# Kernel tuning notes

Measured on AMD Instinct MI355X. Metric: run time of the kernel, lower is better.

The kernel has to match this reference:

```python
import jax, jax.numpy as jnp
import numpy as np

D = 512          # d_model
DS = 32          # d_state
EXPAND = 2
HEADDIM = 64
R = 4            # mimo_rank
DIN = EXPAND * D             # 1024 inner dim
H = DIN // HEADDIM           # 16 heads
DFF = ((int(D * 8 / 3) + 7) // 8) * 8  # 1368 SwiGLU hidden
CHUNK = max(1, 64 // R)      # 16
BATCH, SEQ = 4, 512


def setup_inputs() -> dict:
    key = jax.random.key(0)
    ks = jax.random.split(key, 12)
    def w(k, shape, fan):
        return jax.random.normal(k, shape, jnp.float32) / np.float32(np.sqrt(fan))
    return {
        "x": jax.random.normal(ks[0], (BATCH, SEQ, D), jnp.float32),
        "mask": jnp.ones((BATCH, SEQ), jnp.float32),
        "norm1_w": jnp.ones((D,), jnp.float32),
        "norm2_w": jnp.ones((D,), jnp.float32),
        "Wz": w(ks[1], (D, DIN), D),
        "Wx": w(ks[2], (D, DIN), D),
        "Wb": w(ks[3], (D, H * R * DS), D),
        "Wc": w(ks[4], (D, H * R * DS), D),
        "Wdt": w(ks[5], (D, H), D),
        "dt_bias": jnp.zeros((H,), jnp.float32),
        "A_log": jnp.log(jnp.arange(1, H + 1, dtype=jnp.float32)),
        "D_skip": jnp.ones((H,), jnp.float32),
        "Wout": w(ks[6], (DIN, D), DIN),
        "w1": w(ks[7], (D, DFF), D),
        "w2": w(ks[8], (DFF, D), DFF),
        "w3": w(ks[9], (D, DFF), D),
    }


def rmsnorm(x, wgt, eps=1e-6):
    rms = jnp.sqrt(jnp.mean(x * x, axis=-1, keepdims=True) + eps)
    return x / rms * wgt


def ssm_mixer(x, Wz, Wx, Wb, Wc, Wdt, dt_bias, A_log, D_skip, Wout):
    # x: [B, S, D] (already masked)
    B, S, _ = x.shape
    pad = (CHUNK - S % CHUNK) % CHUNK
    if pad > 0:
        x = jnp.pad(x, ((0, 0), (0, pad), (0, 0)))
    Sp = x.shape[1]
    z = x @ Wz                                        # [B,Sp,DIN] gate
    u = (x @ Wx).reshape(B, Sp, H, HEADDIM)           # [B,Sp,H,P]
    Bm = (x @ Wb).reshape(B, Sp, H, R, DS)            # [B,Sp,H,R,N]
    Cm = (x @ Wc).reshape(B, Sp, H, R, DS)
    dt = jax.nn.softplus(x @ Wdt + dt_bias)           # [B,Sp,H]
    a = jnp.exp(dt * (-jnp.exp(A_log)))               # per-step decay [B,Sp,H]
    ud = u * dt[..., None]                            # discretized input

    def step(h, inp):
        a_t, B_t, C_t, ud_t = inp                     # [B,H], [B,H,R,N], [B,H,R,N], [B,H,P]
        h = a_t[:, :, None, None, None] * h + jnp.einsum('bhrn,bhp->bhrnp', B_t, ud_t)
        y = jnp.einsum('bhrn,bhrnp->bhp', C_t, h)
        return h, y

    h0 = jnp.zeros((B, H, R, DS, HEADDIM), x.dtype)
    xs = (a.swapaxes(0, 1), Bm.swapaxes(0, 1), Cm.swapaxes(0, 1), ud.swapaxes(0, 1))
    _, ys = jax.lax.scan(step, h0, xs)                # ys: [Sp,B,H,P]
    y = ys.swapaxes(0, 1) + u * D_skip[None, None, :, None]
    y = y.reshape(B, Sp, DIN) * jax.nn.silu(z)
    y = y @ Wout                                      # [B,Sp,D]
    return y[:, :S]


def reference(x, mask, norm1_w, norm2_w, Wz, Wx, Wb, Wc, Wdt, dt_bias,
              A_log, D_skip, Wout, w1, w2, w3):
    m = mask[..., None]
    xn = rmsnorm(x, norm1_w) * m
    y = ssm_mixer(xn, Wz, Wx, Wb, Wc, Wdt, dt_bias, A_log, D_skip, Wout) * m
    x = x + y
    xn2 = rmsnorm(x, norm2_w)
    x = x + (jax.nn.silu(xn2 @ w1) * (xn2 @ w3)) @ w2
    return x * m
```

## Files before the change

### kernel.cpp

```cpp
#include <hip/hip_runtime.h>
#include <hip/hip_bf16.h>
#include <math.h>

#define Bn 4
#define Sn 512
#define Dn 512
#define DINn 1024
#define Hn 16
#define Pn 64
#define RNn 128
#define DFFn 1368
#define KP2 1408
#define BSn (Bn*Sn)
#define CH 64
#define NCH (Sn/CH)
#define PSTR 6144
#define FPAD 2816
#define NSCAN (Bn*NCH*Hn)

typedef __attribute__((ext_vector_type(8))) short short8;
typedef __attribute__((ext_vector_type(4))) float f32x4;
typedef __attribute__((ext_vector_type(4))) short short4v;

static __device__ __forceinline__ float bf2f(__hip_bfloat16 v){return __bfloat162float(v);}
static __device__ __forceinline__ __hip_bfloat16 f2bf(float v){return __float2bfloat16(v);}
static __device__ __forceinline__ short f2bfs(float v){ __hip_bfloat16 b=f2bf(v); short s; __builtin_memcpy(&s,&b,2); return s; }
static __device__ __forceinline__ float bfs2f(short s){ __hip_bfloat16 b; __builtin_memcpy(&b,&s,2); return bf2f(b); }

typedef const __attribute__((address_space(1))) unsigned int* gas1_u32p;
typedef __attribute__((address_space(3))) unsigned int* gas3_u32p;
static __device__ __forceinline__ void gl_lds16(const void* g, void* l) {
  __builtin_amdgcn_global_load_lds((gas1_u32p)g, (gas3_u32p)l, 16, 0, 0);
}

struct T8 {
  const float* src[8];
  __hip_bfloat16* dst[8];
  int Rr[8], Cc[8], RrPad[8], CcPad[8], gw[8];
  int start[9];
};

static __device__ __forceinline__ void transpose_tile(const T8& d, int bid, int t,
                                                      float (*tile)[65]) {
  int i = 0;
#pragma unroll
  for (int k = 1; k < 8; ++k) if (bid >= d.start[k]) i = k;
  int rel = bid - d.start[i];
  int gx = rel % d.gw[i], gy = rel / d.gw[i];
  const float* in = d.src[i];
  __hip_bfloat16* out = d.dst[i];
  int Rr = d.Rr[i], Cc = d.Cc[i], RrPad = d.RrPad[i], CcPad = d.CcPad[i];
  int tx = t & 15, ty = t >> 4;
#pragma unroll
  for (int i4 = 0; i4 < 4; ++i4) {
    int r = gy * 64 + ty + i4 * 16;
    int c0 = gx * 64 + tx * 4;
    f32x4 v = (f32x4){0.f, 0.f, 0.f, 0.f};
    if (r < Rr && c0 + 3 < Cc) v = *(const f32x4*)(in + (size_t)r * Cc + c0);
    tile[ty + i4 * 16][tx * 4 + 0] = v[0];
    tile[ty + i4 * 16][tx * 4 + 1] = v[1];
    tile[ty + i4 * 16][tx * 4 + 2] = v[2];
    tile[ty + i4 * 16][tx * 4 + 3] = v[3];
  }
  __syncthreads();
#pragma unroll
  for (int i4 = 0; i4 < 4; ++i4) {
    int r2 = gx * 64 + ty + i4 * 16;
    int c2 = gy * 64 + tx * 4;
    if (r2 < CcPad && c2 + 3 < RrPad) {
      int k = ty + i4 * 16;
      short4v o;
      o.x = f2bfs(tile[tx * 4 + 0][k]);
      o.y = f2bfs(tile[tx * 4 + 1][k]);
      o.z = f2bfs(tile[tx * 4 + 2][k]);
      o.w = f2bfs(tile[tx * 4 + 3][k]);
      *(short4v*)((short*)out + (size_t)r2 * RrPad + c2) = o;
    }
  }
}

__global__ __launch_bounds__(256) void prep_kernel(
    T8 d, const float* __restrict__ x, const float* __restrict__ w,
    const float* __restrict__ mask, const float* __restrict__ Wdt,
    const float* __restrict__ dtb, const float* __restrict__ Alog,
    __hip_bfloat16* __restrict__ outb, float* __restrict__ dt,
    float* __restrict__ la, float* __restrict__ rs, int tstart) {
  __shared__ float tile[64][65];
  __shared__ float xs[Dn];
  __shared__ float red[4];
  int bid = blockIdx.x, t = threadIdx.x;
  if (bid < tstart) {
    transpose_tile(d, bid, t, tile);
  } else if (bid - tstart < BSn) {
    int row = bid - tstart;
    const float* xr = x + (size_t)row * Dn;
    float v0 = xr[t], v1 = xr[t + 256];
    float ss = v0 * v0 + v1 * v1;
#pragma unroll
    for (int o = 32; o > 0; o >>= 1) ss += __shfl_down(ss, o);
    if ((t & 63) == 0) red[t >> 6] = ss;
    __syncthreads();
    float tot = red[0] + red[1] + red[2] + red[3];
    float sc = rsqrtf(tot * (1.f / Dn) + 1e-6f) * mask[row];
    float o0 = v0 * sc * w[t], o1v = v1 * sc * w[t + 256];
    outb[(size_t)row * Dn + t] = f2bf(o0);
    outb[(size_t)row * Dn + t + 256] = f2bf(o1v);
    xs[t] = o0;
    xs[t + 256] = o1v;
    __syncthreads();
    int h = t >> 4, j = t & 15;
    float s = 0.f;
#pragma unroll
    for (int kk = 0; kk < 32; ++kk) {
      int k = j + kk * 16;
      s = fmaf(xs[k], Wdt[k * Hn + h], s);
    }
#pragma unroll
    for (int o = 8; o > 0; o >>= 1) s += __shfl_down(s, o, 16);
    if (j == 0) {
      float v = s + dtb[h];
      float sp = (v > 20.f) ? v : log1pf(expf(v));
      float Ah = expf(Alog[h]);
      dt[(size_t)row * Hn + h] = sp;
      la[(size_t)row * Hn + h] = -Ah * sp;
    }
  } else {
    *(f32x4*)&rs[t * 8]     = (f32x4){0.f, 0.f, 0.f, 0.f};
    *(f32x4*)&rs[t * 8 + 4] = (f32x4){0.f, 0.f, 0.f, 0.f};
  }
}

__global__ __launch_bounds__(256) void gemm_kernel(
    const __hip_bfloat16* __restrict__ A, const __hip_bfloat16* __restrict__ BT,
    __hip_bfloat16* __restrict__ C, int M, int N, int K) {
  __shared__ short As[2][4096];
  __shared__ short Bs[2][4096];
  int m0 = blockIdx.x * 128, n0 = blockIdx.y * 128;
  int t = threadIdx.x;
  int lane = t & 63, wv = t >> 6;
  int wm = (wv & 1) * 64, wn = (wv >> 1) * 64;
  f32x4 acc[4][4];
#pragma unroll
  for (int i = 0; i < 4; ++i)
#pragma unroll
    for (int j = 0; j < 4; ++j) acc[i][j] = (f32x4){0.f, 0.f, 0.f, 0.f};
  const short* Ag = (const short*)A;
  const short* Bg = (const short*)BT;
  int r0 = t >> 2, p = t & 3;
  int q0 = (p - (r0 >> 1)) & 3;
  int r1 = r0 + 64;
  int q1 = (p - (r1 >> 1)) & 3;
  const short* Asrc0 = Ag + (size_t)(m0 + r0) * K + 8 * q0;
  const short* Asrc1 = Ag + (size_t)(m0 + r1) * K + 8 * q1;
  const short* Bsrc0 = Bg + (size_t)(n0 + r0) * K + 8 * q0;
  const short* Bsrc1 = Bg + (size_t)(n0 + r1) * K + 8 * q1;
  int fr = lane & 15, fq = lane >> 4;
  int kTiles = K >> 5;
  auto stage = [&](int buf, int k0) {
    gl_lds16(Asrc0 + k0, &As[buf][wv * 512]);
    gl_lds16(Asrc1 + k0, &As[buf][2048 + wv * 512]);
    gl_lds16(Bsrc0 + k0, &Bs[buf][wv * 512]);
    gl_lds16(Bsrc1 + k0, &Bs[buf][2048 + wv * 512]);
  };
  auto domfma = [&](int buf) {
    short8 af[4], bfr[4];
#pragma unroll
    for (int i = 0; i < 4; ++i) {
      int rr = wm + i * 16 + fr;
      af[i] = *(const short8*)&As[buf][rr * 32 + (((rr >> 1) + fq) & 3) * 8];
    }
#pragma unroll
    for (int i = 0; i < 4; ++i) {
      int rr = wn + i * 16 + fr;
      bfr[i] = *(const short8*)&Bs[buf][rr * 32 + (((rr >> 1) + fq) & 3) * 8];
    }
#pragma unroll
    for (int mi = 0; mi < 4; ++mi)
#pragma unroll
      for (int ni = 0; ni < 4; ++ni)
        acc[mi][ni] = __builtin_amdgcn_mfma_f32_16x16x32_bf16(af[mi], bfr[ni], acc[mi][ni], 0, 0, 0);
  };
  stage(0, 0);
  for (int kt = 0; kt < kTiles; ++kt) {
    int buf = kt & 1;
    __syncthreads();
    if (kt + 1 < kTiles) stage(buf ^ 1, (kt + 1) << 5);
    domfma(buf);
  }
  int fq4 = (lane >> 4) * 4;
#pragma unroll
  for (int mi = 0; mi < 4; ++mi)
#pragma unroll
    for (int ni = 0; ni < 4; ++ni) {
      int col = n0 + wn + ni * 16 + fr;
      if (col < N) {
        int rowb = m0 + wm + mi * 16 + fq4;
#pragma unroll
        for (int r = 0; r < 4; ++r)
          C[(size_t)(rowb + r) * N + col] = f2bf(acc[mi][ni][r]);
      }
    }
}

template <int MODE>
__global__ __launch_bounds__(256) void gemm64_ep_kernel(
    const __hip_bfloat16* __restrict__ A, const __hip_bfloat16* __restrict__ BT,
    const float* __restrict__ aux, const float* __restrict__ mask,
    float* __restrict__ out, float* __restrict__ rs, int M, int N, int K) {
  __shared__ short As[2][64][72];
  __shared__ short Bs[2][64][72];
  int m0 = blockIdx.x * 64, n0 = blockIdx.y * 64;
  int t = threadIdx.x;
  int lane = t & 63, wv = t >> 6;
  int wm = (wv & 1) * 32, wn = (wv >> 1) * 32;
  f32x4 acc[2][2];
#pragma unroll
  for (int i = 0; i < 2; ++i)
#pragma unroll
    for (int j = 0; j < 2; ++j) acc[i][j] = (f32x4){0.f, 0.f, 0.f, 0.f};
  const short* Ag = (const short*)A;
  const short* Bg = (const short*)BT;
  int sr = t >> 2;
  int sc = (t & 3) * 16;
  const short* Ap = Ag + (size_t)(m0 + sr) * K + sc;
  const short* Bp = Bg + (size_t)(n0 + sr) * K + sc;
  int fr = lane & 15, fq = (lane >> 4) * 8;
  int kTiles = K >> 6;
  short8 a0A = 0, a1A = 0, b0A = 0, b1A = 0;
  short8 a0B = 0, a1B = 0, b0B = 0, b1B = 0;
  auto loadA = [&](int k0) {
    a0A = *(const short8*)(Ap + k0);
    a1A = *(const short8*)(Ap + k0 + 8);
    b0A = *(const short8*)(Bp + k0);
    b1A = *(const short8*)(Bp + k0 + 8);
  };
  auto loadB = [&](int k0) {
    a0B = *(const short8*)(Ap + k0);
    a1B = *(const short8*)(Ap + k0 + 8);
    b0B = *(const short8*)(Bp + k0);
    b1B = *(const short8*)(Bp + k0 + 8);
  };
  auto storeA = [&](int buf) {
    *(short8*)&As[buf][sr][sc] = a0A;
    *(short8*)&As[buf][sr][sc + 8] = a1A;
    *(short8*)&Bs[buf][sr][sc] = b0A;
    *(short8*)&Bs[buf][sr][sc + 8] = b1A;
  };
  auto storeB = [&](int buf) {
    *(short8*)&As[buf][sr][sc] = a0B;
    *(short8*)&As[buf][sr][sc + 8] = a1B;
    *(short8*)&Bs[buf][sr][sc] = b0B;
    *(short8*)&Bs[buf][sr][sc + 8] = b1B;
  };
  auto mfma = [&](int buf) {
#pragma unroll
    for (int kk = 0; kk < 2; ++kk) {
      short8 af[2], bfr[2];
#pragma unroll
      for (int i = 0; i < 2; ++i) af[i] = *(const short8*)&As[buf][wm + i * 16 + fr][kk * 32 + fq];
#pragma unroll
      for (int i = 0; i < 2; ++i) bfr[i] = *(const short8*)&Bs[buf][wn + i * 16 + fr][kk * 32 + fq];
#pragma unroll
      for (int mi = 0; mi < 2; ++mi)
#pragma unroll
        for (int ni = 0; ni < 2; ++ni)
          acc[mi][ni] = __builtin_amdgcn_mfma_f32_16x16x32_bf16(af[mi], bfr[ni], acc[mi][ni], 0, 0, 0);
    }
  };
  loadA(0);
  storeA(0);
  loadA(64);
  __syncthreads();
  for (int kt = 0; kt < kTiles; kt += 2) {
    storeA(1);
    if (kt + 2 < kTiles) loadB((kt + 2) << 6);
    mfma(0);
    __syncthreads();
    if (kt + 2 < kTiles) storeB(0);
    if (kt + 3 < kTiles) loadA((kt + 3) << 6);
    mfma(1);
    __syncthreads();
  }
  int fq4 = (lane >> 4) * 4;
  float rsum[2][4];
#pragma unroll
  for (int mi = 0; mi < 2; ++mi)
#pragma unroll
    for (int r = 0; r < 4; ++r) rsum[mi][r] = 0.f;
#pragma unroll
  for (int mi = 0; mi < 2; ++mi)
#pragma unroll
    for (int ni = 0; ni < 2; ++ni) {
      int col = n0 + wn + ni * 16 + fr;
#pragma unroll
      for (int r = 0; r < 4; ++r) {
        int row = m0 + wm + mi * 16 + fq4 + r;
        float m = mask[row];
        size_t a = (size_t)row * N + col;
        float v = acc[mi][ni][r];
        if (MODE == 1) {
          float ov = aux[a] + v * m;
          out[a] = ov;
          rsum[mi][r] += ov * ov;
        } else {
          out[a] = (aux[a] + v) * m;
        }
      }
    }
  if (MODE == 1) {
#pragma unroll
    for (int mi = 0; mi < 2; ++mi)
#pragma unroll
      for (int r = 0; r < 4; ++r) {
        float s = rsum[mi][r];
#pragma unroll
        for (int o = 8; o > 0; o >>= 1) s += __shfl_xor(s, o);
        if ((lane & 15) == 0) {
          int row = m0 + wm + mi * 16 + fq4 + r;
          atomicAdd(&rs[row], s);
        }
      }
  }
}

__global__ __launch_bounds__(256) void gemm64g_kernel(
    const float* __restrict__ X, const float* __restrict__ rs,
    const float* __restrict__ n2w, const __hip_bfloat16* __restrict__ BT,
    __hip_bfloat16* __restrict__ G, int M, int K) {
  __shared__ short As[2][64][72];
  __shared__ short B1s[2][64][72];
  __shared__ short B3s[2][64][72];
  __shared__ float ssc[64];
  __shared__ float sw[Dn];
  int m0 = blockIdx.x * 64, n0 = blockIdx.y * 64;
  int t = threadIdx.x;
  int lane = t & 63, wv = t >> 6;
  int wm = (wv & 1) * 32, wn = (wv >> 1) * 32;
  f32x4 acc1[2][2], acc3[2][2];
#pragma unroll
  for (int i = 0; i < 2; ++i)
#pragma unroll
    for (int j = 0; j < 2; ++j) {
      acc1[i][j] = (f32x4){0.f, 0.f, 0.f, 0.f};
      acc3[i][j] = (f32x4){0.f, 0.f, 0.f, 0.f};
    }
  const short* Bg = (const short*)BT;
  int sr = t >> 2;
  int sc = (t & 3) * 16;
  const float* Xp  = X + (size_t)(m0 + sr) * Dn + sc;
  const short* B1p = Bg + (size_t)(n0 + sr) * K + sc;
  const short* B3p = Bg + (size_t)(DFFn + n0 + sr) * K + sc;
  int fr = lane & 15, fq = (lane >> 4) * 8;
  int kTiles = K >> 6;
  if (t < 64) ssc[t] = rsqrtf(rs[m0 + t] * (1.f / Dn) + 1e-6f);
  sw[t] = n2w[t];
  sw[t + 256] = n2w[t + 256];
  __syncthreads();
  float scl = ssc[sr];
  short8 a0A = 0, a1A = 0, c0A = 0, c1A = 0, d0A = 0, d1A = 0;
  short8 a0B = 0, a1B = 0, c0B = 0, c1B = 0, d0B = 0, d1B = 0;
  auto cvtA = [&](int k0, short8& lo, short8& hi) {
    f32x4 v[4];
#pragma unroll
    for (int q = 0; q < 4; ++q) v[q] = *(const f32x4*)(Xp + k0 + q * 4);
    short tmp[16];
#pragma unroll
    for (int q = 0; q < 4; ++q)
#pragma unroll
      for (int jj = 0; jj < 4; ++jj)
        tmp[q * 4 + jj] = f2bfs(v[q][jj] * scl * sw[k0 + sc + q * 4 + jj]);
    __builtin_memcpy(&lo, tmp, 16);
    __builtin_memcpy(&hi, tmp + 8, 16);
  };
  auto loadA = [&](int k0) {
    cvtA(k0, a0A, a1A);
    c0A = *(const short8*)(B1p + k0);
    c1A = *(const short8*)(B1p + k0 + 8);
    d0A = *(const short8*)(B3p + k0);
    d1A = *(const short8*)(B3p + k0 + 8);
  };
  auto loadB = [&](int k0) {
    cvtA(k0, a0B, a1B);
    c0B = *(const short8*)(B1p + k0);
    c1B = *(const short8*)(B1p + k0 + 8);
    d0B = *(const short8*)(B3p + k0);
    d1B = *(const short8*)(B3p + k0 + 8);
  };
  auto storeA = [&](int buf) {
    *(short8*)&As[buf][sr][sc] = a0A;
    *(short8*)&As[buf][sr][sc + 8] = a1A;
    *(short8*)&B1s[buf][sr][sc] = c0A;
    *(short8*)&B1s[buf][sr][sc + 8] = c1A;
    *(short8*)&B3s[buf][sr][sc] = d0A;
    *(short8*)&B3s[buf][sr][sc + 8] = d1A;
  };
  auto storeB = [&](int buf) {
    *(short8*)&As[buf][sr][sc] = a0B;
    *(short8*)&As[buf][sr][sc + 8] = a1B;
    *(short8*)&B1s[buf][sr][sc] = c0B;
    *(short8*)&B1s[buf][sr][sc + 8] = c1B;
    *(short8*)&B3s[buf][sr][sc] = d0B;
    *(short8*)&B3s[buf][sr][sc + 8] = d1B;
  };
  auto mfma = [&](int buf) {
#pragma unroll
    for (int kk = 0; kk < 2; ++kk) {
      short8 af[2], b1f[2], b3f[2];
#pragma unroll
      for (int i = 0; i < 2; ++i) af[i]  = *(const short8*)&As[buf][wm + i * 16 + fr][kk * 32 + fq];
#pragma unroll
      for (int i = 0; i < 2; ++i) b1f[i] = *(const short8*)&B1s[buf][wn + i * 16 + fr][kk * 32 + fq];
#pragma unroll
      for (int i = 0; i < 2; ++i) b3f[i] = *(const short8*)&B3s[buf][wn + i * 16 + fr][kk * 32 + fq];
#pragma unroll
      for (int mi = 0; mi < 2; ++mi)
#pragma unroll
        for (int ni = 0; ni < 2; ++ni) {
          acc1[mi][ni] = __builtin_amdgcn_mfma_f32_16x16x32_bf16(af[mi], b1f[ni], acc1[mi][ni], 0, 0, 0);
          acc3[mi][ni] = __builtin_amdgcn_mfma_f32_16x16x32_bf16(af[mi], b3f[ni], acc3[mi][ni], 0, 0, 0);
        }
    }
  };
  loadA(0);
  storeA(0);
  loadA(64);
  __syncthreads();
  for (int kt = 0; kt < kTiles; kt += 2) {
    storeA(1);
    if (kt + 2 < kTiles) loadB((kt + 2) << 6);
    mfma(0);
    __syncthreads();
    if (kt + 2 < kTiles) storeB(0);
    if (kt + 3 < kTiles) loadA((kt + 3) << 6);
    mfma(1);
    __syncthreads();
  }
  int fq4 = (lane >> 4) * 4;
#pragma unroll
  for (int mi = 0; mi < 2; ++mi)
#pragma unroll
    for (int ni = 0; ni < 2; ++ni) {
      int col = n0 + wn + ni * 16 + fr;
      bool valid = col < DFFn;
#pragma unroll
      for (int r = 0; r < 4; ++r) {
        int row = m0 + wm + mi * 16 + fq4 + r;
        float h1v = acc1[mi][ni][r];
        float sil = h1v / (1.f + __expf(-h1v));
        float g = sil * acc3[mi][ni][r];
        G[(size_t)row * KP2 + col] = valid ? f2bf(g) : f2bf(0.f);
      }
    }
}

__global__ __launch_bounds__(256) void chunk_intra_kernel(
    const __hip_bfloat16* __restrict__ P, const float* __restrict__ dt,
    const float* __restrict__ la, __hip_bfloat16* __restrict__ ysb,
    __hip_bfloat16* __restrict__ Sbuf, float* __restrict__ ecL, float* __restrict__ ec) {
  int id = blockIdx.x;
  int h = id & 15, c = (id >> 4) & 7, b = id >> 7;
  int t = threadIdx.x, lane = t & 63, wv = t >> 6;
  __shared__ __align__(16) char smem[55040];
  short* sCB = (short*)smem;
  short* sB  = (short*)(smem + 18432);
  short* sUD = (short*)(smem + 35840);
  short* sG  = (short*)(smem + 45056);
  float* scum = (float*)(smem + 54272);
  float* sws  = scum + 64;
  float* sdt  = sws + 64;
  int row0 = b * Sn + c * CH;
  const short* Pb = (const short*)P;
#pragma unroll
  for (int i = 0; i < 4; ++i) {
    int idx = t + i * 256;
    int r = idx >> 4, kk = (idx & 15) * 8;
    *(short8*)&sCB[r * 136 + kk] = *(const short8*)(Pb + (size_t)(row0 + r) * PSTR + 4096 + h * 128 + kk);
    *(short8*)&sB [r * 136 + kk] = *(const short8*)(Pb + (size_t)(row0 + r) * PSTR + 2048 + h * 128 + kk);
  }
  if (t < 64) { sdt[t] = dt[(size_t)(row0 + t) * Hn + h]; scum[t] = la[(size_t)(row0 + t) * Hn + h]; }
  __syncthreads();
  if (wv == 0) {
    float v = scum[lane];
#pragma unroll
    for (int o = 1; o < 64; o <<= 1) { float n = __shfl_up(v, o); if (lane >= o) v += n; }
    scum[lane] = v;
    float c63 = __shfl(v, 63);
    sws[lane] = __expf(c63 - v);
    ec[((size_t)((b * NCH + c) * Hn + h)) * 64 + lane] = __expf(v);
    if (lane == 0) ecL[(b * NCH + c) * Hn + h] = __expf(c63);
  }
#pragma unroll
  for (int i = 0; i < 2; ++i) {
    int idx = t + i * 256;
    int s = idx >> 3, pc = (idx & 7) * 8;
    short8 uv = *(const short8*)(Pb + (size_t)(row0 + s) * PSTR + 1024 + h * 64 + pc);
    float dv = sdt[s];
#pragma unroll
    for (int j = 0; j < 8; ++j) sUD[(pc + j) * 72 + s] = f2bfs(bfs2f(uv[j]) * dv);
  }
  __syncthreads();
  int fr = lane & 15, fq = (lane >> 4) * 8, q4 = (lane >> 4) * 4;
  {
    short8 af[4];
#pragma unroll
    for (int k = 0; k < 4; ++k) af[k] = *(short8*)&sCB[(16 * wv + fr) * 136 + k * 32 + fq];
#pragma unroll
    for (int j = 0; j < 4; ++j) {
      f32x4 acc = (f32x4){0.f, 0.f, 0.f, 0.f};
#pragma unroll
      for (int k = 0; k < 4; ++k) {
        short8 bf = *(short8*)&sB[(16 * j + fr) * 136 + k * 32 + fq];
        acc = __builtin_amdgcn_mfma_f32_16x16x32_bf16(af[k], bf, acc, 0, 0, 0);
      }
      int ss = 16 * j + fr;
      float cs = scum[ss];
#pragma unroll
      for (int r = 0; r < 4; ++r) {
        int tt = 16 * wv + q4 + r;
        float w = (ss <= tt) ? __expf(scum[tt] - cs) : 0.f;
        sG[tt * 72 + ss] = f2bfs(acc[r] * w);
      }
    }
  }
  __syncthreads();
#pragma unroll
  for (int i = 0; i < 32; ++i) {
    int idx = t + i * 256;
    int rn = idx >> 6, s = idx & 63;
    sCB[rn * 72 + s] = f2bfs(bfs2f(sB[s * 136 + rn]) * sws[s]);
  }
  __syncthreads();
  {
    short8 ag[2];
#pragma unroll
    for (int k = 0; k < 2; ++k) ag[k] = *(short8*)&sG[(16 * wv + fr) * 72 + k * 32 + fq];
#pragma unroll
    for (int j = 0; j < 4; ++j) {
      f32x4 acc = (f32x4){0.f, 0.f, 0.f, 0.f};
#pragma unroll
      for (int k = 0; k < 2; ++k) {
        short8 bf = *(short8*)&sUD[(16 * j + fr) * 72 + k * 32 + fq];
        acc = __builtin_amdgcn_mfma_f32_16x16x32_bf16(ag[k], bf, acc, 0, 0, 0);
      }
#pragma unroll
      for (int r = 0; r < 4; ++r)
        ysb[(size_t)(row0 + 16 * wv + q4 + r) * DINn + h * 64 + 16 * j + fr] = f2bf(acc[r]);
    }
  }
#pragma unroll
  for (int mt0 = 0; mt0 < 2; ++mt0) {
    int mt = wv * 2 + mt0;
    short8 ab[2];
#pragma unroll
    for (int k = 0; k < 2; ++k) ab[k] = *(short8*)&sCB[(16 * mt + fr) * 72 + k * 32 + fq];
#pragma unroll
    for (int j = 0; j < 4; ++j) {
      f32x4 acc = (f32x4){0.f, 0.f, 0.f, 0.f};
#pragma unroll
      for (int k = 0; k < 2; ++k) {
        short8 bf = *(short8*)&sUD[(16 * j + fr) * 72 + k * 32 + fq];
        acc = __builtin_amdgcn_mfma_f32_16x16x32_bf16(ab[k], bf, acc, 0, 0, 0);
      }
      int pp = 16 * j + fr;
      int rn0 = 16 * mt + q4;
      short4v o;
      o.x = f2bfs(acc[0]); o.y = f2bfs(acc[1]); o.z = f2bfs(acc[2]); o.w = f2bfs(acc[3]);
      *(short4v*)&((short*)Sbuf)[((size_t)((b * NCH + c) * Hn + h) * 64 + pp) * 128 + rn0] = o;
    }
  }
}

__global__ __launch_bounds__(256) void inter_gate_kernel(
    const __hip_bfloat16* __restrict__ P, const __hip_bfloat16* __restrict__ Sbuf,
    const float* __restrict__ ecL, const float* __restrict__ ec,
    const __hip_bfloat16* __restrict__ ysb, const float* __restrict__ Dsk,
    __hip_bfloat16* __restrict__ y2b) {
  int id = blockIdx.x;
  int h = id & 15, c = (id >> 4) & 7, b = id >> 7;
  int t = threadIdx.x, lane = t & 63, wv = t >> 6;
  __shared__ __align__(16) short sC[64 * 136];
  __shared__ __align__(16) short sHt[64 * 136];
  __shared__ __align__(16) short sz[64 * 64];
  __shared__ __align__(16) short su[64 * 64];
  __shared__ float sec[64];
  int row0 = b * Sn + c * CH;
  const short* Pb = (const short*)P;
#pragma unroll
  for (int i = 0; i < 2; ++i) {
    int idx = t + i * 256;
    int r = idx >> 3, pc = (idx & 7) * 8;
    *(short8*)&sz[r * 64 + pc] = *(const short8*)(Pb + (size_t)(row0 + r) * PSTR + h * 64 + pc);
    *(short8*)&su[r * 64 + pc] = *(const short8*)(Pb + (size_t)(row0 + r) * PSTR + 1024 + h * 64 + pc);
  }
  if (c > 0) {
#pragma unroll
    for (int i = 0; i < 4; ++i) {
      int idx = t + i * 256;
      int r = idx >> 4, kk = (idx & 15) * 8;
      *(short8*)&sC[r * 136 + kk] = *(const short8*)(Pb + (size_t)(row0 + r) * PSTR + 4096 + h * 128 + kk);
    }
    float wch[8];
    {
      float w = 1.f;
      for (int cp = c - 1; cp >= 0; --cp) {
        wch[cp] = w;
        if (cp > 0) w *= ecL[(size_t)((b * NCH + cp) * Hn + h)];
      }
    }
    float hacc[32];
#pragma unroll
    for (int jj = 0; jj < 32; ++jj) hacc[jj] = 0.f;
    const short* Sb = (const short*)Sbuf;
    for (int cp = 0; cp < c; ++cp) {
      size_t base = ((size_t)((b * NCH + cp) * Hn + h)) * 8192 + (size_t)t * 32;
      float wv2 = wch[cp];
#pragma unroll
      for (int v4 = 0; v4 < 4; ++v4) {
        short8 sv = *(const short8*)(Sb + base + v4 * 8);
#pragma unroll
        for (int jj = 0; jj < 8; ++jj)
          hacc[v4 * 8 + jj] = fmaf(wv2, bfs2f(sv[jj]), hacc[v4 * 8 + jj]);
      }
    }
    int p = t >> 2, rn0 = (t & 3) * 32;
#pragma unroll
    for (int v4 = 0; v4 < 4; ++v4) {
      short8 o;
#pragma unroll
      for (int jj = 0; jj < 8; ++jj) o[jj] = f2bfs(hacc[v4 * 8 + jj]);
      *(short8*)&sHt[p * 136 + rn0 + v4 * 8] = o;
    }
    if (t < 64) sec[t] = ec[((size_t)((b * NCH + c) * Hn + h)) * 64 + t];
  }
  __syncthreads();
  int fr = lane & 15, fq = (lane >> 4) * 8, q4 = (lane >> 4) * 4;
  f32x4 acc[4];
#pragma unroll
  for (int j = 0; j < 4; ++j) acc[j] = (f32x4){0.f, 0.f, 0.f, 0.f};
  if (c > 0) {
    short8 af[4];
#pragma unroll
    for (int k = 0; k < 4; ++k) af[k] = *(short8*)&sC[(16 * wv + fr) * 136 + k * 32 + fq];
#pragma unroll
    for (int j = 0; j < 4; ++j)
#pragma unroll
      for (int k = 0; k < 4; ++k) {
        short8 bf = *(short8*)&sHt[(16 * j + fr) * 136 + k * 32 + fq];
        acc[j] = __builtin_amdgcn_mfma_f32_16x16x32_bf16(af[k], bf, acc[j], 0, 0, 0);
      }
  }
  float dsk = Dsk[h];
#pragma unroll
  for (int j = 0; j < 4; ++j) {
    int col = 16 * j + fr;
#pragma unroll
    for (int r = 0; r < 4; ++r) {
      int tt = 16 * wv + q4 + r;
      size_t a = (size_t)(row0 + tt) * DINn + h * 64 + col;
      float val = bf2f(ysb[a]);
      if (c > 0) val += sec[tt] * acc[j][r];
      float uu = bfs2f(su[tt * 64 + col]);
      float zz = bfs2f(sz[tt * 64 + col]);
      float sil = zz / (1.f + __expf(-zz));
      y2b[a] = f2bf((val + uu * dsk) * sil);
    }
  }
}

extern "C" void kernel_launch(void* const* d_in, const int* in_sizes, int n_in,
                              void* d_out, int out_size, void* d_ws, size_t ws_size,
                              hipStream_t stream) {
  const float* x    = (const float*)d_in[0];
  const float* mask = (const float*)d_in[1];
  const float* n1w  = (const float*)d_in[2];
  const float* n2w  = (const float*)d_in[3];
  const float* Wz   = (const float*)d_in[4];
  const float* Wx   = (const float*)d_in[5];
  const float* Wb   = (const float*)d_in[6];
  const float* Wc   = (const float*)d_in[7];
  const float* Wdt  = (const float*)d_in[8];
  const float* dtb  = (const float*)d_in[9];
  const float* Alog = (const float*)d_in[10];
  const float* Dsk  = (const float*)d_in[11];
  const float* Wout = (const float*)d_in[12];
  const float* w1   = (const float*)d_in[13];
  const float* w2   = (const float*)d_in[14];
  const float* w3   = (const float*)d_in[15];

  char* ws = (char*)d_ws;
  size_t off = 0;
  auto alloc = [&](size_t bytes) {
    char* p = ws + off;
    off += (bytes + 255) & ~(size_t)255;
    return p;
  };
  __hip_bfloat16* xnb = (__hip_bfloat16*)alloc((size_t)BSn * Dn * 2);
  __hip_bfloat16* P = (__hip_bfloat16*)alloc((size_t)BSn * PSTR * 2);
  float* dt  = (float*)alloc((size_t)BSn * Hn * 4);
  float* la  = (float*)alloc((size_t)BSn * Hn * 4);
  __hip_bfloat16* ysb = (__hip_bfloat16*)alloc((size_t)BSn * DINn * 2);
  float* ecL = (float*)alloc((size_t)Bn * NCH * Hn * 4);
  float* ec  = (float*)alloc((size_t)Bn * NCH * Hn * 64 * 4);
  float* rs  = (float*)alloc((size_t)BSn * 4);
  __hip_bfloat16* WallT = (__hip_bfloat16*)alloc((size_t)PSTR * Dn * 2);
  __hip_bfloat16* WoutT = (__hip_bfloat16*)alloc((size_t)Dn * DINn * 2);
  __hip_bfloat16* w13T  = (__hip_bfloat16*)alloc((size_t)FPAD * Dn * 2);
  __hip_bfloat16* w2T   = (__hip_bfloat16*)alloc((size_t)Dn * KP2 * 2);
  char* arena = alloc(22000000);
  __hip_bfloat16* Sbuf = (__hip_bfloat16*)arena;
  __hip_bfloat16* y2b  = (__hip_bfloat16*)(arena + 16777216);
  float* xres          = (float*)arena;
  __hip_bfloat16* gatedb = (__hip_bfloat16*)(arena + 4194304);

  T8 td;
  td.src[0] = Wz;   td.dst[0] = WallT;                      td.Rr[0] = 512;  td.Cc[0] = 1024; td.RrPad[0] = 512;  td.CcPad[0] = 1024;
  td.src[1] = Wx;   td.dst[1] = WallT + (size_t)1024 * 512; td.Rr[1] = 512;  td.Cc[1] = 1024; td.RrPad[1] = 512;  td.CcPad[1] = 1024;
  td.src[2] = Wb;   td.dst[2] = WallT + (size_t)2048 * 512; td.Rr[2] = 512;  td.Cc[2] = 2048; td.RrPad[2] = 512;  td.CcPad[2] = 2048;
  td.src[3] = Wc;   td.dst[3] = WallT + (size_t)4096 * 512; td.Rr[3] = 512;  td.Cc[3] = 2048; td.RrPad[3] = 512;  td.CcPad[3] = 2048;
  td.src[4] = Wout; td.dst[4] = WoutT;                      td.Rr[4] = 1024; td.Cc[4] = 512;  td.RrPad[4] = 1024; td.CcPad[4] = 512;
  td.src[5] = w1;   td.dst[5] = w13T;                       td.Rr[5] = 512;  td.Cc[5] = 1368; td.RrPad[5] = 512;  td.CcPad[5] = 1368;
  td.src[6] = w3;   td.dst[6] = w13T + (size_t)1368 * 512;  td.Rr[6] = 512;  td.Cc[6] = 1368; td.RrPad[6] = 512;  td.CcPad[6] = 1448;
  td.src[7] = w2;   td.dst[7] = w2T;                        td.Rr[7] = 1368; td.Cc[7] = 512;  td.RrPad[7] = KP2;  td.CcPad[7] = 512;
  int tot = 0;
  for (int i = 0; i < 8; ++i) {
    td.gw[i] = (td.CcPad[i] + 63) / 64;
    int gh = (td.RrPad[i] + 63) / 64;
    td.start[i] = tot;
    tot += td.gw[i] * gh;
  }
  td.start[8] = tot;

  prep_kernel<<<tot + BSn + 1, 256, 0, stream>>>(td, x, n1w, mask, Wdt, dtb, Alog, xnb, dt, la, rs, tot);
  gemm_kernel<<<dim3(16, 48), 256, 0, stream>>>(xnb, WallT, P, BSn, PSTR, Dn);
  chunk_intra_kernel<<<NSCAN, 256, 0, stream>>>(P, dt, la, ysb, Sbuf, ecL, ec);
  inter_gate_kernel<<<NSCAN, 256, 0, stream>>>(P, Sbuf, ecL, ec, ysb, Dsk, y2b);
  gemm64_ep_kernel<1><<<dim3(32, 8), 256, 0, stream>>>(y2b, WoutT, x, mask, xres, rs, BSn, Dn, DINn);
  gemm64g_kernel<<<dim3(32, KP2 / 64), 256, 0, stream>>>(xres, rs, n2w, w13T, gatedb, BSn, Dn);
  gemm64_ep_kernel<2><<<dim3(32, 8), 256, 0, stream>>>(gatedb, w2T, xres, mask, (float*)d_out, rs, BSn, Dn, KP2);
}
```

Baseline: 212.6 us.

## Fuse chunk scan kernels with flag-based inter-chunk sync and fold norm2 weight into W13

```diff
diff --git a/kernel.cpp b/kernel.cpp
--- a/kernel.cpp
+++ b/kernel.cpp
@@ -35,6 +35,7 @@
 
 struct T8 {
   const float* src[8];
+  const float* svec[8];
   __hip_bfloat16* dst[8];
   int Rr[8], Cc[8], RrPad[8], CcPad[8], gw[8];
   int start[9];
@@ -48,6 +49,7 @@
   int rel = bid - d.start[i];
   int gx = rel % d.gw[i], gy = rel / d.gw[i];
   const float* in = d.src[i];
+  const float* sv = d.svec[i];
   __hip_bfloat16* out = d.dst[i];
   int Rr = d.Rr[i], Cc = d.Cc[i], RrPad = d.RrPad[i], CcPad = d.CcPad[i];
   int tx = t & 15, ty = t >> 4;
@@ -69,11 +71,15 @@
     int c2 = gy * 64 + tx * 4;
     if (r2 < CcPad && c2 + 3 < RrPad) {
       int k = ty + i4 * 16;
+      float s0 = sv ? sv[c2 + 0] : 1.f;
+      float s1 = sv ? sv[c2 + 1] : 1.f;
+      float s2 = sv ? sv[c2 + 2] : 1.f;
+      float s3 = sv ? sv[c2 + 3] : 1.f;
       short4v o;
-      o.x = f2bfs(tile[tx * 4 + 0][k]);
-      o.y = f2bfs(tile[tx * 4 + 1][k]);
-      o.z = f2bfs(tile[tx * 4 + 2][k]);
-      o.w = f2bfs(tile[tx * 4 + 3][k]);
+      o.x = f2bfs(tile[tx * 4 + 0][k] * s0);
+      o.y = f2bfs(tile[tx * 4 + 1][k] * s1);
+      o.z = f2bfs(tile[tx * 4 + 2][k] * s2);
+      o.w = f2bfs(tile[tx * 4 + 3][k] * s3);
       *(short4v*)((short*)out + (size_t)r2 * RrPad + c2) = o;
     }
   }
@@ -84,7 +90,8 @@
     const float* __restrict__ mask, const float* __restrict__ Wdt,
     const float* __restrict__ dtb, const float* __restrict__ Alog,
     __hip_bfloat16* __restrict__ outb, float* __restrict__ dt,
-    float* __restrict__ la, float* __restrict__ rs, int tstart) {
+    float* __restrict__ la, float* __restrict__ rs, int* __restrict__ flags,
+    int tstart) {
   __shared__ float tile[64][65];
   __shared__ float xs[Dn];
   __shared__ float red[4];
@@ -127,6 +134,8 @@
   } else {
     *(f32x4*)&rs[t * 8]     = (f32x4){0.f, 0.f, 0.f, 0.f};
     *(f32x4*)&rs[t * 8 + 4] = (f32x4){0.f, 0.f, 0.f, 0.f};
+    ((int2*)flags)[t] = make_int2(0, 0);
+    if (t < 4) flags[512 + t] = 0;
   }
 }
 
@@ -206,7 +215,8 @@
 __global__ __launch_bounds__(256) void gemm64_ep_kernel(
     const __hip_bfloat16* __restrict__ A, const __hip_bfloat16* __restrict__ BT,
     const float* __restrict__ aux, const float* __restrict__ mask,
-    float* __restrict__ out, float* __restrict__ rs, int M, int N, int K) {
+    float* __restrict__ out, __hip_bfloat16* __restrict__ outb,
+    float* __restrict__ rs, int M, int N, int K) {
   __shared__ short As[2][64][72];
   __shared__ short Bs[2][64][72];
   int m0 = blockIdx.x * 64, n0 = blockIdx.y * 64;
@@ -301,6 +311,7 @@
         if (MODE == 1) {
           float ov = aux[a] + v * m;
           out[a] = ov;
+          outb[a] = f2bf(ov);
           rsum[mi][r] += ov * ov;
         } else {
           out[a] = (aux[a] + v) * m;
@@ -324,14 +335,13 @@
 }
 
 __global__ __launch_bounds__(256) void gemm64g_kernel(
-    const float* __restrict__ X, const float* __restrict__ rs,
-    const float* __restrict__ n2w, const __hip_bfloat16* __restrict__ BT,
-    __hip_bfloat16* __restrict__ G, int M, int K) {
+    const __hip_bfloat16* __restrict__ A, const float* __restrict__ rs,
+    const __hip_bfloat16* __restrict__ BT, __hip_bfloat16* __restrict__ G,
+    int M, int K) {
   __shared__ short As[2][64][72];
   __shared__ short B1s[2][64][72];
   __shared__ short B3s[2][64][72];
   __shared__ float ssc[64];
-  __shared__ float sw[Dn];
   int m0 = blockIdx.x * 64, n0 = blockIdx.y * 64;
   int t = threadIdx.x;
   int lane = t & 63, wv = t >> 6;
@@ -344,43 +354,29 @@
       acc1[i][j] = (f32x4){0.f, 0.f, 0.f, 0.f};
       acc3[i][j] = (f32x4){0.f, 0.f, 0.f, 0.f};
     }
+  const short* Ag = (const short*)A;
   const short* Bg = (const short*)BT;
   int sr = t >> 2;
   int sc = (t & 3) * 16;
-  const float* Xp  = X + (size_t)(m0 + sr) * Dn + sc;
+  const short* Ap  = Ag + (size_t)(m0 + sr) * K + sc;
   const short* B1p = Bg + (size_t)(n0 + sr) * K + sc;
   const short* B3p = Bg + (size_t)(DFFn + n0 + sr) * K + sc;
   int fr = lane & 15, fq = (lane >> 4) * 8;
   int kTiles = K >> 6;
   if (t < 64) ssc[t] = rsqrtf(rs[m0 + t] * (1.f / Dn) + 1e-6f);
-  sw[t] = n2w[t];
-  sw[t + 256] = n2w[t + 256];
-  __syncthreads();
-  float scl = ssc[sr];
   short8 a0A = 0, a1A = 0, c0A = 0, c1A = 0, d0A = 0, d1A = 0;
   short8 a0B = 0, a1B = 0, c0B = 0, c1B = 0, d0B = 0, d1B = 0;
-  auto cvtA = [&](int k0, short8& lo, short8& hi) {
-    f32x4 v[4];
-#pragma unroll
-    for (int q = 0; q < 4; ++q) v[q] = *(const f32x4*)(Xp + k0 + q * 4);
-    short tmp[16];
-#pragma unroll
-    for (int q = 0; q < 4; ++q)
-#pragma unroll
-      for (int jj = 0; jj < 4; ++jj)
-        tmp[q * 4 + jj] = f2bfs(v[q][jj] * scl * sw[k0 + sc + q * 4 + jj]);
-    __builtin_memcpy(&lo, tmp, 16);
-    __builtin_memcpy(&hi, tmp + 8, 16);
-  };
   auto loadA = [&](int k0) {
-    cvtA(k0, a0A, a1A);
+    a0A = *(const short8*)(Ap + k0);
+    a1A = *(const short8*)(Ap + k0 + 8);
     c0A = *(const short8*)(B1p + k0);
     c1A = *(const short8*)(B1p + k0 + 8);
     d0A = *(const short8*)(B3p + k0);
     d1A = *(const short8*)(B3p + k0 + 8);
   };
   auto loadB = [&](int k0) {
-    cvtA(k0, a0B, a1B);
+    a0B = *(const short8*)(Ap + k0);
+    a1B = *(const short8*)(Ap + k0 + 8);
     c0B = *(const short8*)(B1p + k0);
     c1B = *(const short8*)(B1p + k0 + 8);
     d0B = *(const short8*)(B3p + k0);
@@ -444,30 +440,41 @@
       bool valid = col < DFFn;
 #pragma unroll
       for (int r = 0; r < 4; ++r) {
-        int row = m0 + wm + mi * 16 + fq4 + r;
-        float h1v = acc1[mi][ni][r];
+        int rloc = wm + mi * 16 + fq4 + r;
+        float scl = ssc[rloc];
+        float h1v = acc1[mi][ni][r] * scl;
         float sil = h1v / (1.f + __expf(-h1v));
-        float g = sil * acc3[mi][ni][r];
-        G[(size_t)row * KP2 + col] = valid ? f2bf(g) : f2bf(0.f);
+        float g = sil * (acc3[mi][ni][r] * scl);
+        G[(size_t)(m0 + rloc) * KP2 + col] = valid ? f2bf(g) : f2bf(0.f);
       }
     }
 }
 
-__global__ __launch_bounds__(256) void chunk_intra_kernel(
+__global__ __launch_bounds__(256) void scan_fused_kernel(
     const __hip_bfloat16* __restrict__ P, const float* __restrict__ dt,
-    const float* __restrict__ la, __hip_bfloat16* __restrict__ ysb,
-    __hip_bfloat16* __restrict__ Sbuf, float* __restrict__ ecL, float* __restrict__ ec) {
-  int id = blockIdx.x;
-  int h = id & 15, c = (id >> 4) & 7, b = id >> 7;
-  int t = threadIdx.x, lane = t & 63, wv = t >> 6;
-  __shared__ __align__(16) char smem[55040];
-  short* sCB = (short*)smem;
-  short* sB  = (short*)(smem + 18432);
-  short* sUD = (short*)(smem + 35840);
-  short* sG  = (short*)(smem + 45056);
-  float* scum = (float*)(smem + 54272);
+    const float* __restrict__ la, __hip_bfloat16* __restrict__ Sbuf,
+    float* __restrict__ ecL, int* __restrict__ flags,
+    const float* __restrict__ Dsk, __hip_bfloat16* __restrict__ y2b) {
+  __shared__ __align__(16) char smem[72448];
+  __shared__ int swid;
+  short* sCB  = (short*)smem;
+  short* sB   = (short*)(smem + 17408);
+  short* sUD  = (short*)(smem + 34816);
+  short* sG   = (short*)(smem + 44032);
+  short* sBwT = (short*)(smem + 53248);
+  float* scum = (float*)(smem + 71680);
   float* sws  = scum + 64;
   float* sdt  = sws + 64;
+  short* sz  = sB;
+  short* su  = sB + 8192;
+  short* sHt = sBwT;
+  int t = threadIdx.x, lane = t & 63, wv = t >> 6;
+  int* counter = flags + 512;
+  if (t == 0) swid = atomicAdd(counter, 1);
+  __syncthreads();
+  int id = swid;
+  int h = id & 15, c = (id >> 4) & 7, b = id >> 7;
+  int fi = (b * NCH + c) * Hn + h;
   int row0 = b * Sn + c * CH;
   const short* Pb = (const short*)P;
 #pragma unroll
@@ -486,8 +493,7 @@
     scum[lane] = v;
     float c63 = __shfl(v, 63);
     sws[lane] = __expf(c63 - v);
-    ec[((size_t)((b * NCH + c) * Hn + h)) * 64 + lane] = __expf(v);
-    if (lane == 0) ecL[(b * NCH + c) * Hn + h] = __expf(c63);
+    if (lane == 0) ecL[fi] = __expf(c63);
   }
 #pragma unroll
   for (int i = 0; i < 2; ++i) {
@@ -499,7 +505,36 @@
     for (int j = 0; j < 8; ++j) sUD[(pc + j) * 72 + s] = f2bfs(bfs2f(uv[j]) * dv);
   }
   __syncthreads();
+#pragma unroll
+  for (int i = 0; i < 32; ++i) {
+    int idx = t + i * 256;
+    int rn = idx >> 6, s = idx & 63;
+    sBwT[rn * 72 + s] = f2bfs(bfs2f(sB[s * 136 + rn]) * sws[s]);
+  }
+  __syncthreads();
   int fr = lane & 15, fq = (lane >> 4) * 8, q4 = (lane >> 4) * 4;
+#pragma unroll
+  for (int mt0 = 0; mt0 < 2; ++mt0) {
+    int mt = wv * 2 + mt0;
+    short8 ab[2];
+#pragma unroll
+    for (int k = 0; k < 2; ++k) ab[k] = *(short8*)&sBwT[(16 * mt + fr) * 72 + k * 32 + fq];
+#pragma unroll
+    for (int j = 0; j < 4; ++j) {
+      f32x4 acc = (f32x4){0.f, 0.f, 0.f, 0.f};
+#pragma unroll
+      for (int k = 0; k < 2; ++k) {
+        short8 bfv = *(short8*)&sUD[(16 * j + fr) * 72 + k * 32 + fq];
+        acc = __builtin_amdgcn_mfma_f32_16x16x32_bf16(ab[k], bfv, acc, 0, 0, 0);
+      }
+      int pp = 16 * j + fr;
+      int rn0 = 16 * mt + q4;
+      short4v o;
+      o.x = f2bfs(acc[0]); o.y = f2bfs(acc[1]); o.z = f2bfs(acc[2]); o.w = f2bfs(acc[3]);
+      *(short4v*)&((short*)Sbuf)[((size_t)fi * 64 + pp) * 128 + rn0] = o;
+    }
+  }
+  f32x4 ysr[4];
   {
     short8 af[4];
 #pragma unroll
@@ -509,8 +544,8 @@
       f32x4 acc = (f32x4){0.f, 0.f, 0.f, 0.f};
 #pragma unroll
       for (int k = 0; k < 4; ++k) {
-        short8 bf = *(short8*)&sB[(16 * j + fr) * 136 + k * 32 + fq];
-        acc = __builtin_amdgcn_mfma_f32_16x16x32_bf16(af[k], bf, acc, 0, 0, 0);
+        short8 bfv = *(short8*)&sB[(16 * j + fr) * 136 + k * 32 + fq];
+        acc = __builtin_amdgcn_mfma_f32_16x16x32_bf16(af[k], bfv, acc, 0, 0, 0);
       }
       int ss = 16 * j + fr;
       float cs = scum[ss];
@@ -523,13 +558,10 @@
     }
   }
   __syncthreads();
-#pragma unroll
-  for (int i = 0; i < 32; ++i) {
-    int idx = t + i * 256;
-    int rn = idx >> 6, s = idx & 63;
-    sCB[rn * 72 + s] = f2bfs(bfs2f(sB[s * 136 + rn]) * sws[s]);
-  }
-  __syncthreads();
+  if (t == 0) {
+    __threadfence();
+    __hip_atomic_store(&flags[fi], 1, __ATOMIC_RELEASE, __HIP_MEMORY_SCOPE_AGENT);
+  }
   {
     short8 ag[2];
 #pragma unroll
@@ -539,52 +571,13 @@
       f32x4 acc = (f32x4){0.f, 0.f, 0.f, 0.f};
 #pragma unroll
       for (int k = 0; k < 2; ++k) {
-        short8 bf = *(short8*)&sUD[(16 * j + fr) * 72 + k * 32 + fq];
-        acc = __builtin_amdgcn_mfma_f32_16x16x32_bf16(ag[k], bf, acc, 0, 0, 0);
-      }
-#pragma unroll
-      for (int r = 0; r < 4; ++r)
-        ysb[(size_t)(row0 + 16 * wv + q4 + r) * DINn + h * 64 + 16 * j + fr] = f2bf(acc[r]);
-    }
-  }
-#pragma unroll
-  for (int mt0 = 0; mt0 < 2; ++mt0) {
-    int mt = wv * 2 + mt0;
-    short8 ab[2];
-#pragma unroll
-    for (int k = 0; k < 2; ++k) ab[k] = *(short8*)&sCB[(16 * mt + fr) * 72 + k * 32 + fq];
-#pragma unroll
-    for (int j = 0; j < 4; ++j) {
-      f32x4 acc = (f32x4){0.f, 0.f, 0.f, 0.f};
-#pragma unroll
-      for (int k = 0; k < 2; ++k) {
-        short8 bf = *(short8*)&sUD[(16 * j + fr) * 72 + k * 32 + fq];
-        acc = __builtin_amdgcn_mfma_f32_16x16x32_bf16(ab[k], bf, acc, 0, 0, 0);
-      }
-      int pp = 16 * j + fr;
-      int rn0 = 16 * mt + q4;
-      short4v o;
-      o.x = f2bfs(acc[0]); o.y = f2bfs(acc[1]); o.z = f2bfs(acc[2]); o.w = f2bfs(acc[3]);
-      *(short4v*)&((short*)Sbuf)[((size_t)((b * NCH + c) * Hn + h) * 64 + pp) * 128 + rn0] = o;
-    }
-  }
-}
-
-__global__ __launch_bounds__(256) void inter_gate_kernel(
-    const __hip_bfloat16* __restrict__ P, const __hip_bfloat16* __restrict__ Sbuf,
-    const float* __restrict__ ecL, const float* __restrict__ ec,
-    const __hip_bfloat16* __restrict__ ysb, const float* __restrict__ Dsk,
-    __hip_bfloat16* __restrict__ y2b) {
-  int id = blockIdx.x;
-  int h = id & 15, c = (id >> 4) & 7, b = id >> 7;
-  int t = threadIdx.x, lane = t & 63, wv = t >> 6;
-  __shared__ __align__(16) short sC[64 * 136];
-  __shared__ __align__(16) short sHt[64 * 136];
-  __shared__ __align__(16) short sz[64 * 64];
-  __shared__ __align__(16) short su[64 * 64];
-  __shared__ float sec[64];
-  int row0 = b * Sn + c * CH;
-  const short* Pb = (const short*)P;
+        short8 bfv = *(short8*)&sUD[(16 * j + fr) * 72 + k * 32 + fq];
+        acc = __builtin_amdgcn_mfma_f32_16x16x32_bf16(ag[k], bfv, acc, 0, 0, 0);
+      }
+      ysr[j] = acc;
+    }
+  }
+  __syncthreads();
 #pragma unroll
   for (int i = 0; i < 2; ++i) {
     int idx = t + i * 256;
@@ -593,60 +586,53 @@
     *(short8*)&su[r * 64 + pc] = *(const short8*)(Pb + (size_t)(row0 + r) * PSTR + 1024 + h * 64 + pc);
   }
   if (c > 0) {
-#pragma unroll
-    for (int i = 0; i < 4; ++i) {
-      int idx = t + i * 256;
-      int r = idx >> 4, kk = (idx & 15) * 8;
-      *(short8*)&sC[r * 136 + kk] = *(const short8*)(Pb + (size_t)(row0 + r) * PSTR + 4096 + h * 128 + kk);
-    }
-    float wch[8];
-    {
-      float w = 1.f;
-      for (int cp = c - 1; cp >= 0; --cp) {
-        wch[cp] = w;
-        if (cp > 0) w *= ecL[(size_t)((b * NCH + cp) * Hn + h)];
-      }
-    }
+    if (t == 0) {
+      for (int cp = 0; cp < c; ++cp) {
+        int fj = (b * NCH + cp) * Hn + h;
+        while (__hip_atomic_load(&flags[fj], __ATOMIC_ACQUIRE, __HIP_MEMORY_SCOPE_AGENT) == 0)
+          __builtin_amdgcn_s_sleep(8);
+      }
+    }
+    __syncthreads();
     float hacc[32];
 #pragma unroll
     for (int jj = 0; jj < 32; ++jj) hacc[jj] = 0.f;
     const short* Sb = (const short*)Sbuf;
-    for (int cp = 0; cp < c; ++cp) {
+    float wrun = 1.f;
+    for (int cp = c - 1; cp >= 0; --cp) {
       size_t base = ((size_t)((b * NCH + cp) * Hn + h)) * 8192 + (size_t)t * 32;
-      float wv2 = wch[cp];
 #pragma unroll
       for (int v4 = 0; v4 < 4; ++v4) {
         short8 sv = *(const short8*)(Sb + base + v4 * 8);
 #pragma unroll
         for (int jj = 0; jj < 8; ++jj)
-          hacc[v4 * 8 + jj] = fmaf(wv2, bfs2f(sv[jj]), hacc[v4 * 8 + jj]);
-      }
-    }
-    int p = t >> 2, rn0 = (t & 3) * 32;
+          hacc[v4 * 8 + jj] = fmaf(wrun, bfs2f(sv[jj]), hacc[v4 * 8 + jj]);
+      }
+      wrun *= ecL[(size_t)((b * NCH + cp) * Hn + h)];
+    }
+    int pp = t >> 2, rn0 = (t & 3) * 32;
 #pragma unroll
     for (int v4 = 0; v4 < 4; ++v4) {
       short8 o;
 #pragma unroll
       for (int jj = 0; jj < 8; ++jj) o[jj] = f2bfs(hacc[v4 * 8 + jj]);
-      *(short8*)&sHt[p * 136 + rn0 + v4 * 8] = o;
-    }
-    if (t < 64) sec[t] = ec[((size_t)((b * NCH + c) * Hn + h)) * 64 + t];
-  }
-  __syncthreads();
-  int fr = lane & 15, fq = (lane >> 4) * 8, q4 = (lane >> 4) * 4;
+      *(short8*)&sHt[pp * 136 + rn0 + v4 * 8] = o;
+    }
+  }
+  __syncthreads();
   f32x4 acc[4];
 #pragma unroll
   for (int j = 0; j < 4; ++j) acc[j] = (f32x4){0.f, 0.f, 0.f, 0.f};
   if (c > 0) {
     short8 af[4];
 #pragma unroll
-    for (int k = 0; k < 4; ++k) af[k] = *(short8*)&sC[(16 * wv + fr) * 136 + k * 32 + fq];
+    for (int k = 0; k < 4; ++k) af[k] = *(short8*)&sCB[(16 * wv + fr) * 136 + k * 32 + fq];
 #pragma unroll
     for (int j = 0; j < 4; ++j)
 #pragma unroll
       for (int k = 0; k < 4; ++k) {
-        short8 bf = *(short8*)&sHt[(16 * j + fr) * 136 + k * 32 + fq];
-        acc[j] = __builtin_amdgcn_mfma_f32_16x16x32_bf16(af[k], bf, acc[j], 0, 0, 0);
+        short8 bfv = *(short8*)&sHt[(16 * j + fr) * 136 + k * 32 + fq];
+        acc[j] = __builtin_amdgcn_mfma_f32_16x16x32_bf16(af[k], bfv, acc[j], 0, 0, 0);
       }
   }
   float dsk = Dsk[h];
@@ -657,8 +643,8 @@
     for (int r = 0; r < 4; ++r) {
       int tt = 16 * wv + q4 + r;
       size_t a = (size_t)(row0 + tt) * DINn + h * 64 + col;
-      float val = bf2f(ysb[a]);
-      if (c > 0) val += sec[tt] * acc[j][r];
+      float val = ysr[j][r];
+      if (c > 0) val += __expf(scum[tt]) * acc[j][r];
       float uu = bfs2f(su[tt * 64 + col]);
       float zz = bfs2f(sz[tt * 64 + col]);
       float sil = zz / (1.f + __expf(-zz));
@@ -698,21 +684,22 @@
   __hip_bfloat16* P = (__hip_bfloat16*)alloc((size_t)BSn * PSTR * 2);
   float* dt  = (float*)alloc((size_t)BSn * Hn * 4);
   float* la  = (float*)alloc((size_t)BSn * Hn * 4);
-  __hip_bfloat16* ysb = (__hip_bfloat16*)alloc((size_t)BSn * DINn * 2);
   float* ecL = (float*)alloc((size_t)Bn * NCH * Hn * 4);
-  float* ec  = (float*)alloc((size_t)Bn * NCH * Hn * 64 * 4);
   float* rs  = (float*)alloc((size_t)BSn * 4);
+  int* flags = (int*)alloc(516 * 4);
   __hip_bfloat16* WallT = (__hip_bfloat16*)alloc((size_t)PSTR * Dn * 2);
   __hip_bfloat16* WoutT = (__hip_bfloat16*)alloc((size_t)Dn * DINn * 2);
   __hip_bfloat16* w13T  = (__hip_bfloat16*)alloc((size_t)FPAD * Dn * 2);
   __hip_bfloat16* w2T   = (__hip_bfloat16*)alloc((size_t)Dn * KP2 * 2);
-  char* arena = alloc(22000000);
+  char* arena = alloc(23200000);
   __hip_bfloat16* Sbuf = (__hip_bfloat16*)arena;
   __hip_bfloat16* y2b  = (__hip_bfloat16*)(arena + 16777216);
   float* xres          = (float*)arena;
   __hip_bfloat16* gatedb = (__hip_bfloat16*)(arena + 4194304);
+  __hip_bfloat16* xresb  = (__hip_bfloat16*)(arena + 20971520);
 
   T8 td;
+  for (int i = 0; i < 8; ++i) td.svec[i] = nullptr;
   td.src[0] = Wz;   td.dst[0] = WallT;                      td.Rr[0] = 512;  td.Cc[0] = 1024; td.RrPad[0] = 512;  td.CcPad[0] = 1024;
   td.src[1] = Wx;   td.dst[1] = WallT + (size_t)1024 * 512; td.Rr[1] = 512;  td.Cc[1] = 1024; td.RrPad[1] = 512;  td.CcPad[1] = 1024;
   td.src[2] = Wb;   td.dst[2] = WallT + (size_t)2048 * 512; td.Rr[2] = 512;  td.Cc[2] = 2048; td.RrPad[2] = 512;  td.CcPad[2] = 2048;
@@ -721,6 +708,8 @@
   td.src[5] = w1;   td.dst[5] = w13T;                       td.Rr[5] = 512;  td.Cc[5] = 1368; td.RrPad[5] = 512;  td.CcPad[5] = 1368;
   td.src[6] = w3;   td.dst[6] = w13T + (size_t)1368 * 512;  td.Rr[6] = 512;  td.Cc[6] = 1368; td.RrPad[6] = 512;  td.CcPad[6] = 1448;
   td.src[7] = w2;   td.dst[7] = w2T;                        td.Rr[7] = 1368; td.Cc[7] = 512;  td.RrPad[7] = KP2;  td.CcPad[7] = 512;
+  td.svec[5] = n2w;
+  td.svec[6] = n2w;
   int tot = 0;
   for (int i = 0; i < 8; ++i) {
     td.gw[i] = (td.CcPad[i] + 63) / 64;
@@ -730,11 +719,10 @@
   }
   td.start[8] = tot;
 
-  prep_kernel<<<tot + BSn + 1, 256, 0, stream>>>(td, x, n1w, mask, Wdt, dtb, Alog, xnb, dt, la, rs, tot);
+  prep_kernel<<<tot + BSn + 1, 256, 0, stream>>>(td, x, n1w, mask, Wdt, dtb, Alog, xnb, dt, la, rs, flags, tot);
   gemm_kernel<<<dim3(16, 48), 256, 0, stream>>>(xnb, WallT, P, BSn, PSTR, Dn);
-  chunk_intra_kernel<<<NSCAN, 256, 0, stream>>>(P, dt, la, ysb, Sbuf, ecL, ec);
-  inter_gate_kernel<<<NSCAN, 256, 0, stream>>>(P, Sbuf, ecL, ec, ysb, Dsk, y2b);
-  gemm64_ep_kernel<1><<<dim3(32, 8), 256, 0, stream>>>(y2b, WoutT, x, mask, xres, rs, BSn, Dn, DINn);
-  gemm64g_kernel<<<dim3(32, KP2 / 64), 256, 0, stream>>>(xres, rs, n2w, w13T, gatedb, BSn, Dn);
-  gemm64_ep_kernel<2><<<dim3(32, 8), 256, 0, stream>>>(gatedb, w2T, xres, mask, (float*)d_out, rs, BSn, Dn, KP2);
+  scan_fused_kernel<<<NSCAN, 256, 0, stream>>>(P, dt, la, Sbuf, ecL, flags, Dsk, y2b);
+  gemm64_ep_kernel<1><<<dim3(32, 8), 256, 0, stream>>>(y2b, WoutT, x, mask, xres, xresb, rs, BSn, Dn, DINn);
+  gemm64g_kernel<<<dim3(32, KP2 / 64), 256, 0, stream>>>(xresb, rs, w13T, gatedb, BSn, Dn);
+  gemm64_ep_kernel<2><<<dim3(32, 8), 256, 0, stream>>>(gatedb, w2T, xres, mask, (float*)d_out, nullptr, rs, BSn, Dn, KP2);
 }
```

New measurement: 262.9 us. 1.24x slower.
